# Kernel tuning notes

Measured on AMD Instinct MI355X. Metric: run time of the kernel, lower is better.

Reference implementation:

```python
import jax, jax.numpy as jnp
import numpy as np

N, G, C, A, E = 10000, 12, 64, 3, 50000
LN_EPS = 1e-5


def setup_inputs() -> dict:
    key = jax.random.key(0)
    ks = jax.random.split(key, 12)
    s = 0.05
    return {
        "x": jax.random.normal(ks[0], (N, G, C), jnp.float32),
        "edge_attr": jax.random.normal(ks[1], (E, G, G, A), jnp.float32),
        "W_kernel": jax.random.normal(ks[2], (A, C), jnp.float32) * s,   # depthwise kernel basis Linear(attr_dim->C)
        "conv_bias": jax.random.normal(ks[3], (C,), jnp.float32) * s,
        "ln_w": jnp.ones((C,), jnp.float32),
        "ln_b": jnp.zeros((C,), jnp.float32),
        "W1": jax.random.normal(ks[4], (C, C), jnp.float32) * s,          # stored [in,out]
        "b1": jax.random.normal(ks[5], (C,), jnp.float32) * s,
        "W2": jax.random.normal(ks[6], (C, C), jnp.float32) * s,
        "b2": jax.random.normal(ks[7], (C,), jnp.float32) * s,
        "layer_scale": jnp.full((1, C), 1e-6, jnp.float32),
        "edge_index": jax.random.randint(ks[8], (2, E), 0, N, jnp.int32),
        "batch": jnp.zeros((N,), jnp.int32),
    }


def reference(x, edge_attr, W_kernel, conv_bias, ln_w, ln_b, W1, b1, W2, b2,
              layer_scale, edge_index, batch):
    src, dst = edge_index[0], edge_index[1]
    x_j = x[src]                                            # [E,G,C] gather
    # depthwise fiber conv: m[e,g,c] = sum_{h,a} attr[e,g,h,a] * Wk[a,c] * x_j[e,h,c]
    # contract over source grid h first to avoid materializing the [E,G,G,C] kernel
    t = jnp.einsum('egha,ehc->egac', edge_attr, x_j)        # [E,G,A,C]
    m = jnp.einsum('egac,ac->egc', t, W_kernel)             # [E,G,C]
    agg = jnp.zeros_like(x).at[dst].add(m) + conv_bias      # scatter-add, [N,G,C]
    # LayerNorm over channel dim
    mu = jnp.mean(agg, axis=-1, keepdims=True)
    var = jnp.mean(jnp.square(agg - mu), axis=-1, keepdims=True)
    h = (agg - mu) * jax.lax.rsqrt(var + LN_EPS) * ln_w + ln_b
    # 2-layer MLP with exact GELU (torch default)
    h = jax.nn.gelu(h @ W1 + b1, approximate=False) @ W2 + b2
    h = layer_scale * h                                     # broadcast [1,C] over [N,G,C]
    return x + h                                            # residual (same shape)
```

## Files before the change

kernel.cpp:

```cpp
#include <hip/hip_runtime.h>
#include <math.h>

#define NN 10000
#define GG 12
#define CC 64
#define AA 3
#define EE 50000
#define LN_EPS 1e-5f
#define MAXDEG 64

typedef __attribute__((ext_vector_type(4))) float f4;
typedef __attribute__((ext_vector_type(4))) short s4;

union S4U { s4 s; unsigned int w[2]; };

__device__ __forceinline__ s4 pack4(float k0, float k1, float k2, float k3) {
    S4U t;
    t.w[0] = __builtin_amdgcn_perm(__float_as_uint(k1), __float_as_uint(k0), 0x07060302u);
    t.w[1] = __builtin_amdgcn_perm(__float_as_uint(k3), __float_as_uint(k2), 0x07060302u);
    return t.s;
}

__device__ __forceinline__ f4 mfma_bf16(s4 a, s4 b, f4 c) {
#if __has_builtin(__builtin_amdgcn_mfma_f32_16x16x16bf16_1k)
    return __builtin_amdgcn_mfma_f32_16x16x16bf16_1k(a, b, c, 0, 0, 0);
#else
    asm volatile("v_mfma_f32_16x16x16_bf16 %0, %1, %2, %0" : "+v"(c) : "v"(a), "v"(b));
    return c;
#endif
}

__global__ __launch_bounds__(256) void zero_cnt(int* __restrict__ cnt) {
    int i = blockIdx.x * 256 + threadIdx.x;
    if (i < NN) cnt[i] = 0;
}

__global__ __launch_bounds__(256) void bucket_fill(const int* __restrict__ ei,
                                                   int* __restrict__ cnt,
                                                   int* __restrict__ elist) {
    int e = blockIdx.x * 256 + threadIdx.x;
    if (e < EE) {
        int src = ei[e];
        int dst = ei[EE + e];
        int pos = atomicAdd(&cnt[dst], 1);
        if (pos < MAXDEG) elist[dst * MAXDEG + pos] = e | (src << 17);
    }
}

__global__ __launch_bounds__(256) void conv_mfma(
    const float* __restrict__ x, const float* __restrict__ attr,
    const float* __restrict__ Wk,
    const int* __restrict__ cnt, const int* __restrict__ elist,
    float* __restrict__ agg) {
    const int l  = threadIdx.x & 63;
    const int wv = threadIdx.x >> 6;
    const int n  = blockIdx.x * 4 + wv;
    const int lm = l & 15;
    const int lg = l >> 4;

    int aoff[3];
#pragma unroll
    for (int a = 0; a < 3; ++a)
        aoff[a] = (lm < 12 && lg < 3) ? (lm * 144 + lg * 48 + a * 4) : 0;
    const int boff = (lg < 3) ? (lg * 1024 + lm * 4) : 0;
    const unsigned bmsk = (lg < 3) ? 0xFFFFFFFFu : 0u;

    const int deg = min(cnt[n], MAXDEG);
    const int myE = elist[n * MAXDEG + l];

    f4 acc[3][4];
#pragma unroll
    for (int a = 0; a < 3; ++a)
#pragma unroll
        for (int t = 0; t < 4; ++t) acc[a][t] = (f4){0.f, 0.f, 0.f, 0.f};

    for (int i = 0; i < deg; ++i) {
        const int p   = __builtin_amdgcn_readlane(myE, i);
        const int e   = p & 0x1FFFF;
        const int src = p >> 17;
        const char* ab = (const char*)(attr + (size_t)e * (GG * GG * AA));
        const char* xb = (const char*)(x + src * (GG * CC));

        float ar[3][4];
#pragma unroll
        for (int a = 0; a < 3; ++a) {
            const char* pa = ab + aoff[a];
#pragma unroll
            for (int j = 0; j < 4; ++j)
                ar[a][j] = *(const float*)(pa + j * 12);
        }
        float br[4][4];
#pragma unroll
        for (int t = 0; t < 4; ++t) {
            const char* pb = xb + boff + t * 64;
#pragma unroll
            for (int j = 0; j < 4; ++j)
                br[t][j] = *(const float*)(pb + j * 256);
        }

        s4 af[3], bf[4];
#pragma unroll
        for (int a = 0; a < 3; ++a)
            af[a] = pack4(ar[a][0], ar[a][1], ar[a][2], ar[a][3]);
#pragma unroll
        for (int t = 0; t < 4; ++t) {
            S4U u; u.s = pack4(br[t][0], br[t][1], br[t][2], br[t][3]);
            u.w[0] &= bmsk; u.w[1] &= bmsk;
            bf[t] = u.s;
        }

#pragma unroll
        for (int a = 0; a < 3; ++a)
#pragma unroll
            for (int t = 0; t < 4; ++t)
                acc[a][t] = mfma_bf16(af[a], bf[t], acc[a][t]);
    }

    float wk[3][4];
#pragma unroll
    for (int a = 0; a < 3; ++a)
#pragma unroll
        for (int t = 0; t < 4; ++t)
            wk[a][t] = Wk[a * CC + lm + 16 * t];

    float* ob = agg + n * (GG * CC);
    if (lg < 3) {
#pragma unroll
        for (int t = 0; t < 4; ++t) {
#pragma unroll
            for (int r = 0; r < 4; ++r) {
                const float m = fmaf(acc[0][t][r], wk[0][t],
                                fmaf(acc[1][t][r], wk[1][t],
                                     acc[2][t][r] * wk[2][t]));
                ob[(lg * 4 + r) * CC + lm + 16 * t] = m;
            }
        }
    }
}

__global__ __launch_bounds__(256) void ln_mlp_mfma(
    const float* __restrict__ x, const float* __restrict__ cb,
    const float* __restrict__ lnw, const float* __restrict__ lnb,
    const float* __restrict__ W1, const float* __restrict__ b1,
    const float* __restrict__ W2, const float* __restrict__ b2,
    const float* __restrict__ ls, float* __restrict__ out) {
    __shared__ float sbuf[4][16 * 68];

    const int l  = threadIdx.x & 63;
    const int wv = threadIdx.x >> 6;
    const int lm = l & 15;
    const int lg = l >> 4;
    const int f0 = (blockIdx.x * 4 + wv) * 16;

    const float* aggp = out + (size_t)(f0 + lm) * CC + 4 * lg;
    f4 h4[4];
#pragma unroll
    for (int kt = 0; kt < 4; ++kt) h4[kt] = *(const f4*)(aggp + 16 * kt);

    f4 cb4[4], lw4[4], lb4[4];
#pragma unroll
    for (int kt = 0; kt < 4; ++kt) {
        cb4[kt] = *(const f4*)(cb  + 4 * lg + 16 * kt);
        lw4[kt] = *(const f4*)(lnw + 4 * lg + 16 * kt);
        lb4[kt] = *(const f4*)(lnb + 4 * lg + 16 * kt);
    }

    float s = 0.f, s2 = 0.f;
#pragma unroll
    for (int kt = 0; kt < 4; ++kt)
#pragma unroll
        for (int j = 0; j < 4; ++j) {
            const float v = h4[kt][j] + cb4[kt][j];
            h4[kt][j] = v;
            s += v; s2 += v * v;
        }
    s  += __shfl_xor(s, 16);  s  += __shfl_xor(s, 32);
    s2 += __shfl_xor(s2, 16); s2 += __shfl_xor(s2, 32);
    const float mu  = s * (1.f / 64.f);
    const float inv = rsqrtf(s2 * (1.f / 64.f) - mu * mu + LN_EPS);

    s4 hf[4];
#pragma unroll
    for (int kt = 0; kt < 4; ++kt) {
        const float n0 = (h4[kt][0] - mu) * inv * lw4[kt][0] + lb4[kt][0];
        const float n1 = (h4[kt][1] - mu) * inv * lw4[kt][1] + lb4[kt][1];
        const float n2 = (h4[kt][2] - mu) * inv * lw4[kt][2] + lb4[kt][2];
        const float n3 = (h4[kt][3] - mu) * inv * lw4[kt][3] + lb4[kt][3];
        hf[kt] = pack4(n0, n1, n2, n3);
    }

    s4 w1f[4][4];
#pragma unroll
    for (int mt = 0; mt < 4; ++mt)
#pragma unroll
        for (int kt = 0; kt < 4; ++kt) {
            const int kb = 4 * lg + 16 * kt;
            const int m  = lm + 16 * mt;
            w1f[mt][kt] = pack4(W1[(kb + 0) * CC + m], W1[(kb + 1) * CC + m],
                                W1[(kb + 2) * CC + m], W1[(kb + 3) * CC + m]);
        }

    f4 z[4];
#pragma unroll
    for (int mt = 0; mt < 4; ++mt) z[mt] = (f4){0.f, 0.f, 0.f, 0.f};
#pragma unroll
    for (int mt = 0; mt < 4; ++mt)
#pragma unroll
        for (int kt = 0; kt < 4; ++kt)
            z[mt] = mfma_bf16(w1f[mt][kt], hf[kt], z[mt]);

    s4 gf[4];
#pragma unroll
    for (int mt = 0; mt < 4; ++mt) {
        const f4 b14 = *(const f4*)(b1 + 16 * mt + 4 * lg);
        float g[4];
#pragma unroll
        for (int r = 0; r < 4; ++r) {
            const float zz = z[mt][r] + b14[r];
            g[r] = 0.5f * zz * (1.f + erff(zz * 0.70710678118654752f));
        }
        gf[mt] = pack4(g[0], g[1], g[2], g[3]);
    }

    s4 w2f[4][4];
#pragma unroll
    for (int mt = 0; mt < 4; ++mt)
#pragma unroll
        for (int kt = 0; kt < 4; ++kt) {
            const int kb = 4 * lg + 16 * kt;
            const int m  = lm + 16 * mt;
            w2f[mt][kt] = pack4(W2[(kb + 0) * CC + m], W2[(kb + 1) * CC + m],
                                W2[(kb + 2) * CC + m], W2[(kb + 3) * CC + m]);
        }

    f4 o[4];
#pragma unroll
    for (int mt = 0; mt < 4; ++mt) o[mt] = (f4){0.f, 0.f, 0.f, 0.f};
#pragma unroll
    for (int mt = 0; mt < 4; ++mt)
#pragma unroll
        for (int kt = 0; kt < 4; ++kt)
            o[mt] = mfma_bf16(w2f[mt][kt], gf[kt], o[mt]);

    float* sb = sbuf[wv];
    const int fbase = lm * 68;
    const int swz   = (l & 7) << 2;
#pragma unroll
    for (int mt = 0; mt < 4; ++mt)
#pragma unroll
        for (int r = 0; r < 4; ++r)
            sb[fbase + ((16 * mt + 4 * lg + r) ^ swz)] = o[mt][r];

    const f4 b2q = *(const f4*)(b2 + 4 * lm);
    const f4 lsq = *(const f4*)(ls + 4 * lm);

#pragma unroll
    for (int rr = 0; rr < 4; ++rr) {
        const int R   = rr * 4 + lg;
        const int col = 4 * lm;
        const f4 ov = *(const f4*)(&sb[R * 68 + (col ^ ((R & 7) << 2))]);
        const f4 xv = *(const f4*)(x + (size_t)(f0 + R) * CC + col);
        f4 res;
#pragma unroll
        for (int k = 0; k < 4; ++k)
            res[k] = fmaf(lsq[k], ov[k] + b2q[k], xv[k]);
        *(f4*)(out + (size_t)(f0 + R) * CC + col) = res;
    }
}

extern "C" void kernel_launch(void* const* d_in, const int* in_sizes, int n_in,
                              void* d_out, int out_size, void* d_ws, size_t ws_size,
                              hipStream_t stream) {
    const float* x    = (const float*)d_in[0];
    const float* attr = (const float*)d_in[1];
    const float* Wk   = (const float*)d_in[2];
    const float* cb   = (const float*)d_in[3];
    const float* lnw  = (const float*)d_in[4];
    const float* lnb  = (const float*)d_in[5];
    const float* W1   = (const float*)d_in[6];
    const float* b1   = (const float*)d_in[7];
    const float* W2   = (const float*)d_in[8];
    const float* b2   = (const float*)d_in[9];
    const float* ls   = (const float*)d_in[10];
    const int*   ei   = (const int*)d_in[11];
    float* out = (float*)d_out;

    int* cnt   = (int*)d_ws;
    int* elist = cnt + NN;

    zero_cnt<<<(NN + 255) / 256, 256, 0, stream>>>(cnt);
    bucket_fill<<<(EE + 255) / 256, 256, 0, stream>>>(ei, cnt, elist);
    conv_mfma<<<NN / 4, 256, 0, stream>>>(x, attr, Wk, cnt, elist, out);
    ln_mlp_mfma<<<1875, 256, 0, stream>>>(x, cb, lnw, lnb, W1, b1, W2, b2, ls, out);
}
```

Measured before the change: 81.68 us.

## Stage edge attributes through LDS with coalesced loads and prefetch next edge

Edge attributes are now loaded with coalesced 16-byte vector loads into a per-wave double-buffered LDS slab and read back with three vector LDS reads per lane. This replaces the twelve strided scalar global loads per lane. The x rows and attributes for the next edge are prefetched in registers while the current edge's MFMAs run, to hide global memory latency. The cost is extra LDS traffic and register pressure. It also relies on wave-level ordering of LDS writes and reads without an explicit barrier.

```diff
diff --git a/kernel.cpp b/kernel.cpp
--- a/kernel.cpp
+++ b/kernel.cpp
@@ -52,18 +52,18 @@
     const float* __restrict__ Wk,
     const int* __restrict__ cnt, const int* __restrict__ elist,
     float* __restrict__ agg) {
+    __shared__ float lsa[4][2][432];
+
     const int l  = threadIdx.x & 63;
     const int wv = threadIdx.x >> 6;
     const int n  = blockIdx.x * 4 + wv;
     const int lm = l & 15;
     const int lg = l >> 4;
 
-    int aoff[3];
-#pragma unroll
-    for (int a = 0; a < 3; ++a)
-        aoff[a] = (lm < 12 && lg < 3) ? (lm * 144 + lg * 48 + a * 4) : 0;
     const int boff = (lg < 3) ? (lg * 1024 + lm * 4) : 0;
     const unsigned bmsk = (lg < 3) ? 0xFFFFFFFFu : 0u;
+    const int fbase = (lm < 12 && lg < 3) ? (lm * 36 + lg * 12) : 0;
+    const int a1l   = (l < 44) ? l : 43;
 
     const int deg = min(cnt[n], MAXDEG);
     const int myE = elist[n * MAXDEG + l];
@@ -74,40 +74,58 @@
 #pragma unroll
         for (int t = 0; t < 4; ++t) acc[a][t] = (f4){0.f, 0.f, 0.f, 0.f};
 
+    f4 A0, A1;
+    float xr[16];
+
+    if (deg > 0) {
+        const int p   = __builtin_amdgcn_readlane(myE, 0);
+        const char* ab = (const char*)(attr + (size_t)(p & 0x1FFFF) * (GG * GG * AA));
+        const char* xb = (const char*)(x + (p >> 17) * (GG * CC));
+        A0 = *(const f4*)(ab + 16 * l);
+        A1 = *(const f4*)(ab + 1024 + 16 * a1l);
+#pragma unroll
+        for (int t = 0; t < 4; ++t)
+#pragma unroll
+            for (int j = 0; j < 4; ++j)
+                xr[4 * t + j] = *(const float*)(xb + boff + t * 64 + j * 256);
+    }
+
     for (int i = 0; i < deg; ++i) {
-        const int p   = __builtin_amdgcn_readlane(myE, i);
-        const int e   = p & 0x1FFFF;
-        const int src = p >> 17;
-        const char* ab = (const char*)(attr + (size_t)e * (GG * GG * AA));
-        const char* xb = (const char*)(x + src * (GG * CC));
-
-        float ar[3][4];
-#pragma unroll
-        for (int a = 0; a < 3; ++a) {
-            const char* pa = ab + aoff[a];
-#pragma unroll
-            for (int j = 0; j < 4; ++j)
-                ar[a][j] = *(const float*)(pa + j * 12);
-        }
-        float br[4][4];
+        float* sw = &lsa[wv][i & 1][0];
+
+        *(f4*)(sw + 4 * l) = A0;
+        if (l < 44) *(f4*)(sw + 256 + 4 * l) = A1;
+
+        s4 bf[4];
 #pragma unroll
         for (int t = 0; t < 4; ++t) {
-            const char* pb = xb + boff + t * 64;
-#pragma unroll
-            for (int j = 0; j < 4; ++j)
-                br[t][j] = *(const float*)(pb + j * 256);
-        }
-
-        s4 af[3], bf[4];
-#pragma unroll
-        for (int a = 0; a < 3; ++a)
-            af[a] = pack4(ar[a][0], ar[a][1], ar[a][2], ar[a][3]);
-#pragma unroll
-        for (int t = 0; t < 4; ++t) {
-            S4U u; u.s = pack4(br[t][0], br[t][1], br[t][2], br[t][3]);
+            S4U u; u.s = pack4(xr[4 * t], xr[4 * t + 1], xr[4 * t + 2], xr[4 * t + 3]);
             u.w[0] &= bmsk; u.w[1] &= bmsk;
             bf[t] = u.s;
         }
+
+        if (i + 1 < deg) {
+            const int p   = __builtin_amdgcn_readlane(myE, i + 1);
+            const char* ab = (const char*)(attr + (size_t)(p & 0x1FFFF) * (GG * GG * AA));
+            const char* xb = (const char*)(x + (p >> 17) * (GG * CC));
+            A0 = *(const f4*)(ab + 16 * l);
+            A1 = *(const f4*)(ab + 1024 + 16 * a1l);
+#pragma unroll
+            for (int t = 0; t < 4; ++t)
+#pragma unroll
+                for (int j = 0; j < 4; ++j)
+                    xr[4 * t + j] = *(const float*)(xb + boff + t * 64 + j * 256);
+        }
+
+        const float* sr = sw + fbase;
+        const f4 q0 = *(const f4*)(sr);
+        const f4 q1 = *(const f4*)(sr + 4);
+        const f4 q2 = *(const f4*)(sr + 8);
+
+        s4 af[3];
+        af[0] = pack4(q0[0], q0[3], q1[2], q2[1]);
+        af[1] = pack4(q0[1], q1[0], q1[3], q2[2]);
+        af[2] = pack4(q0[2], q1[1], q2[0], q2[3]);
 
 #pragma unroll
         for (int a = 0; a < 3; ++a)
```

Result: faster. 77.45 us (-5.2%).

## Prepack x to bf16 MFMA layout, stage edge attrs via LDS with prefetch

Applied to the files above, without the earlier changes.

Adds an xpack kernel that converts x into bf16 fragments already laid out per lane for the MFMA B operand, so the gather loop reads two 16-byte vectors per lane instead of 16 scattered scalar loads and skips repacking per edge. Edge attributes are now read with coalesced 16-byte loads into a double-buffered shared-memory slot and re-read per lane to build A fragments. The next edge's loads are issued before the current compute. The conv kernel moves to one wave per block. This costs an extra kernel launch, an extra workspace buffer, and LDS round trips.

```diff
diff --git a/kernel.cpp b/kernel.cpp
--- a/kernel.cpp
+++ b/kernel.cpp
@@ -13,12 +13,16 @@
 typedef __attribute__((ext_vector_type(4))) short s4;
 
 union S4U { s4 s; unsigned int w[2]; };
+union I2S { int i[2]; s4 s; };
 
 __device__ __forceinline__ s4 pack4(float k0, float k1, float k2, float k3) {
     S4U t;
     t.w[0] = __builtin_amdgcn_perm(__float_as_uint(k1), __float_as_uint(k0), 0x07060302u);
     t.w[1] = __builtin_amdgcn_perm(__float_as_uint(k3), __float_as_uint(k2), 0x07060302u);
     return t.s;
+}
+__device__ __forceinline__ unsigned int pack2(float a, float b) {
+    return __builtin_amdgcn_perm(__float_as_uint(b), __float_as_uint(a), 0x07060302u);
 }
 
 __device__ __forceinline__ f4 mfma_bf16(s4 a, s4 b, f4 c) {
@@ -47,23 +51,48 @@
     }
 }
 
-__global__ __launch_bounds__(256) void conv_mfma(
-    const float* __restrict__ x, const float* __restrict__ attr,
+__global__ __launch_bounds__(256) void xpack(const float* __restrict__ x,
+                                             unsigned int* __restrict__ xp) {
+    const int l  = threadIdx.x & 63;
+    const int n  = blockIdx.x * 4 + (threadIdx.x >> 6);
+    const int lm = l & 15;
+    const int lg = l >> 4;
+
+    unsigned int d[8];
+    if (lg < 3) {
+        const char* xb = (const char*)(x + n * (GG * CC)) + lg * 1024 + lm * 4;
+#pragma unroll
+        for (int t = 0; t < 4; ++t) {
+            const float v0 = *(const float*)(xb + t * 64 + 0 * 256);
+            const float v1 = *(const float*)(xb + t * 64 + 1 * 256);
+            const float v2 = *(const float*)(xb + t * 64 + 2 * 256);
+            const float v3 = *(const float*)(xb + t * 64 + 3 * 256);
+            d[2 * t]     = pack2(v0, v1);
+            d[2 * t + 1] = pack2(v2, v3);
+        }
+    } else {
+#pragma unroll
+        for (int k = 0; k < 8; ++k) d[k] = 0u;
+    }
+    unsigned int* o = xp + (size_t)n * 512 + l * 8;
+    *(uint4*)o       = make_uint4(d[0], d[1], d[2], d[3]);
+    *(uint4*)(o + 4) = make_uint4(d[4], d[5], d[6], d[7]);
+}
+
+__global__ __launch_bounds__(64) void conv_mfma(
+    const unsigned int* __restrict__ xp, const float* __restrict__ attr,
     const float* __restrict__ Wk,
     const int* __restrict__ cnt, const int* __restrict__ elist,
     float* __restrict__ agg) {
-    const int l  = threadIdx.x & 63;
-    const int wv = threadIdx.x >> 6;
-    const int n  = blockIdx.x * 4 + wv;
+    __shared__ float lsa[2][432];
+
+    const int l  = threadIdx.x;
+    const int n  = blockIdx.x;
     const int lm = l & 15;
     const int lg = l >> 4;
 
-    int aoff[3];
-#pragma unroll
-    for (int a = 0; a < 3; ++a)
-        aoff[a] = (lm < 12 && lg < 3) ? (lm * 144 + lg * 48 + a * 4) : 0;
-    const int boff = (lg < 3) ? (lg * 1024 + lm * 4) : 0;
-    const unsigned bmsk = (lg < 3) ? 0xFFFFFFFFu : 0u;
+    const int fbase = (lm < 12 && lg < 3) ? (lm * 36 + lg * 12) : 0;
+    const int a1l   = (l < 44) ? l : 43;
 
     const int deg = min(cnt[n], MAXDEG);
     const int myE = elist[n * MAXDEG + l];
@@ -74,47 +103,74 @@
 #pragma unroll
         for (int t = 0; t < 4; ++t) acc[a][t] = (f4){0.f, 0.f, 0.f, 0.f};
 
-    for (int i = 0; i < deg; ++i) {
-        const int p   = __builtin_amdgcn_readlane(myE, i);
-        const int e   = p & 0x1FFFF;
-        const int src = p >> 17;
-        const char* ab = (const char*)(attr + (size_t)e * (GG * GG * AA));
-        const char* xb = (const char*)(x + src * (GG * CC));
-
-        float ar[3][4];
-#pragma unroll
-        for (int a = 0; a < 3; ++a) {
-            const char* pa = ab + aoff[a];
-#pragma unroll
-            for (int j = 0; j < 4; ++j)
-                ar[a][j] = *(const float*)(pa + j * 12);
-        }
-        float br[4][4];
-#pragma unroll
-        for (int t = 0; t < 4; ++t) {
-            const char* pb = xb + boff + t * 64;
-#pragma unroll
-            for (int j = 0; j < 4; ++j)
-                br[t][j] = *(const float*)(pb + j * 256);
-        }
-
-        s4 af[3], bf[4];
-#pragma unroll
-        for (int a = 0; a < 3; ++a)
-            af[a] = pack4(ar[a][0], ar[a][1], ar[a][2], ar[a][3]);
-#pragma unroll
-        for (int t = 0; t < 4; ++t) {
-            S4U u; u.s = pack4(br[t][0], br[t][1], br[t][2], br[t][3]);
-            u.w[0] &= bmsk; u.w[1] &= bmsk;
-            bf[t] = u.s;
-        }
-
-#pragma unroll
-        for (int a = 0; a < 3; ++a)
-#pragma unroll
-            for (int t = 0; t < 4; ++t)
-                acc[a][t] = mfma_bf16(af[a], bf[t], acc[a][t]);
-    }
+    f4 Aa0, Aa1, Ab0, Ab1;
+    int4 Xa0, Xa1, Xb0, Xb1;
+
+#define LOADE(idx, A0, A1, X0, X1)                                              \
+    {                                                                           \
+        const int p = __builtin_amdgcn_readlane(myE, (idx));                    \
+        const char* ab = (const char*)(attr + (size_t)(p & 0x1FFFF) * 432);     \
+        A0 = *(const f4*)(ab + 16 * l);                                         \
+        A1 = *(const f4*)(ab + 1024 + 16 * a1l);                                \
+        const int* xb = (const int*)(xp + (size_t)(p >> 17) * 512 + 8 * l);     \
+        X0 = *(const int4*)xb;                                                  \
+        X1 = *(const int4*)(xb + 4);                                            \
+    }
+
+#define STAGE(slot, A0, A1)                                                     \
+    {                                                                           \
+        float* sw = &lsa[slot][0];                                              \
+        *(f4*)(sw + 4 * l) = A0;                                                \
+        if (l < 44) *(f4*)(sw + 256 + 4 * l) = A1;                              \
+    }
+
+#define COMPUTE(slot, X0, X1)                                                   \
+    {                                                                           \
+        I2S u0, u1, u2, u3;                                                     \
+        u0.i[0] = X0.x; u0.i[1] = X0.y;                                         \
+        u1.i[0] = X0.z; u1.i[1] = X0.w;                                         \
+        u2.i[0] = X1.x; u2.i[1] = X1.y;                                         \
+        u3.i[0] = X1.z; u3.i[1] = X1.w;                                         \
+        const float* sr = &lsa[slot][0] + fbase;                                \
+        const f4 q0 = *(const f4*)(sr);                                         \
+        const f4 q1 = *(const f4*)(sr + 4);                                     \
+        const f4 q2 = *(const f4*)(sr + 8);                                     \
+        const s4 af0 = pack4(q0[0], q0[3], q1[2], q2[1]);                       \
+        const s4 af1 = pack4(q0[1], q1[0], q1[3], q2[2]);                       \
+        const s4 af2 = pack4(q0[2], q1[1], q2[0], q2[3]);                       \
+        acc[0][0] = mfma_bf16(af0, u0.s, acc[0][0]);                            \
+        acc[1][0] = mfma_bf16(af1, u0.s, acc[1][0]);                            \
+        acc[2][0] = mfma_bf16(af2, u0.s, acc[2][0]);                            \
+        acc[0][1] = mfma_bf16(af0, u1.s, acc[0][1]);                            \
+        acc[1][1] = mfma_bf16(af1, u1.s, acc[1][1]);                            \
+        acc[2][1] = mfma_bf16(af2, u1.s, acc[2][1]);                            \
+        acc[0][2] = mfma_bf16(af0, u2.s, acc[0][2]);                            \
+        acc[1][2] = mfma_bf16(af1, u2.s, acc[1][2]);                            \
+        acc[2][2] = mfma_bf16(af2, u2.s, acc[2][2]);                            \
+        acc[0][3] = mfma_bf16(af0, u3.s, acc[0][3]);                            \
+        acc[1][3] = mfma_bf16(af1, u3.s, acc[1][3]);                            \
+        acc[2][3] = mfma_bf16(af2, u3.s, acc[2][3]);                            \
+    }
+
+    if (deg > 0) LOADE(0, Aa0, Aa1, Xa0, Xa1);
+    if (deg > 1) LOADE(1, Ab0, Ab1, Xb0, Xb1);
+    if (deg > 0) STAGE(0, Aa0, Aa1);
+
+    for (int i = 0; i < deg; i += 2) {
+        if (i + 2 < deg) LOADE(i + 2, Aa0, Aa1, Xa0, Xa1);
+        COMPUTE(0, Xa0, Xa1);
+        if (i + 1 < deg) STAGE(1, Ab0, Ab1);
+
+        if (i + 1 < deg) {
+            COMPUTE(1, Xb0, Xb1);
+            if (i + 3 < deg) LOADE(i + 3, Ab0, Ab1, Xb0, Xb1);
+            if (i + 2 < deg) STAGE(0, Aa0, Aa1);
+        }
+    }
+
+#undef LOADE
+#undef STAGE
+#undef COMPUTE
 
     float wk[3][4];
 #pragma unroll
@@ -123,7 +179,7 @@
         for (int t = 0; t < 4; ++t)
             wk[a][t] = Wk[a * CC + lm + 16 * t];
 
-    float* ob = agg + n * (GG * CC);
+    float* ob = agg + (size_t)n * (GG * CC);
     if (lg < 3) {
 #pragma unroll
         for (int t = 0; t < 4; ++t) {
@@ -287,9 +343,11 @@
 
     int* cnt   = (int*)d_ws;
     int* elist = cnt + NN;
+    unsigned int* xp = (unsigned int*)(elist + NN * MAXDEG);
 
     zero_cnt<<<(NN + 255) / 256, 256, 0, stream>>>(cnt);
     bucket_fill<<<(EE + 255) / 256, 256, 0, stream>>>(ei, cnt, elist);
-    conv_mfma<<<NN / 4, 256, 0, stream>>>(x, attr, Wk, cnt, elist, out);
+    xpack<<<NN / 4, 256, 0, stream>>>(x, xp);
+    conv_mfma<<<NN, 64, 0, stream>>>(xp, attr, Wk, cnt, elist, out);
     ln_mlp_mfma<<<1875, 256, 0, stream>>>(x, cb, lnw, lnb, W1, b1, W2, b2, ls, out);
 }
```

Measured after the change: 79.32 us. -2.9%, faster.
